# Optimization experiments

Measured on AMD Instinct MI355X. Metric: run time of the kernel, lower is better.

## Reference

```python
import jax, jax.numpy as jnp
import numpy as np

N_NODES = 100000
N_EDGES = 1600000
IN_SIZE = 256
OUT_SIZE = 64


def setup_inputs() -> dict:
    key = jax.random.key(0)
    k1, k2, k3 = jax.random.split(key, 3)
    edge_index = jax.random.randint(k1, (2, N_EDGES), 0, N_NODES, dtype=jnp.int32)
    x = jax.random.normal(k2, (N_NODES, IN_SIZE), dtype=jnp.float32)
    W = jax.random.normal(k3, (OUT_SIZE, IN_SIZE), dtype=jnp.float32) * 0.05
    return {"edge_index": edge_index, "x": x, "num_nodes": N_NODES, "W": W}


def reference(edge_index, x, num_nodes, W):
    row, col = edge_index[0], edge_index[1]
    # fill_diag(adj, 1.0): drop any existing diagonal entries (value -> 0),
    # then add exactly one self-loop per node with value 1.0.
    val = jnp.where(row == col, 0.0, 1.0).astype(x.dtype)
    loops = jnp.arange(num_nodes, dtype=row.dtype)
    row_f = jnp.concatenate([row, loops])
    col_f = jnp.concatenate([col, loops])
    val_f = jnp.concatenate([val, jnp.ones((num_nodes,), dtype=x.dtype)])
    # deg = row-sum of adjacency values; D^{-1/2} with inf -> 0
    deg = jax.ops.segment_sum(val_f, row_f, num_segments=num_nodes)
    dinv = jnp.where(deg > 0, deg ** -0.5, 0.0)
    # edge weight: d^{-1/2}[row] * a * d^{-1/2}[col]
    norm = dinv[row_f] * val_f * dinv[col_f]
    # dense projection then SpMM aggregation
    xw = x @ W.T  # [N, out]
    msgs = norm[:, None] * xw[col_f]  # gather over edges [E+N, out]
    out = jax.ops.segment_sum(msgs, row_f, num_segments=num_nodes)
    return out
```

## Files before the change

kernel.cpp:

```cpp
#include <hip/hip_runtime.h>

#define IN_SIZE 256
#define OUT_SIZE 64
#define BSHIFT 7
#define BROWS 128
#define BMASK 127
#define CAP 2560
#define K1_TILE 4096

typedef __attribute__((ext_vector_type(8))) short short8;
typedef __attribute__((ext_vector_type(4))) float floatx4;

__device__ inline unsigned short f2bf(float f) {
  unsigned u = __builtin_bit_cast(unsigned, f);
  u += 0x7fff + ((u >> 16) & 1);
  return (unsigned short)(u >> 16);
}
__device__ inline float bf2f(unsigned short u) {
  unsigned v = (unsigned)u << 16;
  return __builtin_bit_cast(float, v);
}

__global__ __launch_bounds__(256) void wconv_kernel(const float* __restrict__ W,
                                                    unsigned short* __restrict__ Wb,
                                                    int* __restrict__ coarse_cursor,
                                                    int total, int nbuck) {
  int i = blockIdx.x * 256 + threadIdx.x;
  if (i < total) Wb[i] = f2bf(W[i]);
  if (i < nbuck) coarse_cursor[i] = 0;
}

__global__ __launch_bounds__(256) void bucket_coarse_kernel(
    const int* __restrict__ row, const int* __restrict__ col,
    int* __restrict__ coarse_cursor, unsigned* __restrict__ pairs,
    int n_edges, int nbuck) {
  __shared__ int hist[1024];
  int tid = threadIdx.x;
#pragma unroll
  for (int i = 0; i < 4; i++) hist[tid + i * 256] = 0;
  __syncthreads();

  int r[16], c[16];
  int ebase = blockIdx.x * K1_TILE + tid;
#pragma unroll
  for (int i = 0; i < 16; i++) {
    int e = ebase + i * 256;
    bool ok = e < n_edges;
    r[i] = ok ? row[e] : -1;
    c[i] = ok ? col[e] : -1;
    if (ok && r[i] != c[i]) atomicAdd(&hist[r[i] >> BSHIFT], 1);
  }
  __syncthreads();

  for (int i = tid; i < nbuck; i += 256) {
    int cnt = hist[i];
    if (cnt) hist[i] = atomicAdd(&coarse_cursor[i], cnt);
  }
  __syncthreads();

#pragma unroll
  for (int i = 0; i < 16; i++) {
    if (r[i] >= 0 && r[i] != c[i]) {
      int bin = r[i] >> BSHIFT;
      int slot = atomicAdd(&hist[bin], 1);
      if (slot < CAP)
        pairs[(size_t)bin * CAP + slot] =
            ((unsigned)(r[i] & BMASK) << 17) | (unsigned)c[i];
    }
  }
}

__global__ __launch_bounds__(256) void bucket_fine_kernel(
    const int* __restrict__ coarse_cursor, const unsigned* __restrict__ pairs,
    unsigned* __restrict__ colsp, int* __restrict__ count,
    int* __restrict__ row_start, float* __restrict__ dinv, int n_nodes) {
  __shared__ unsigned lpair[CAP];
  __shared__ int hist[BROWS];
  __shared__ int scn[BROWS];
  int tid = threadIdx.x;
  int b = blockIdx.x;
  size_t base = (size_t)b * CAP;
  int n_b = coarse_cursor[b];
  if (n_b > CAP) n_b = CAP;

  if (tid < BROWS) hist[tid] = 0;
  __syncthreads();

  for (int i = tid; i < n_b; i += 256) {
    unsigned p = pairs[base + i];
    lpair[i] = p;
    atomicAdd(&hist[p >> 17], 1);
  }
  __syncthreads();

  if (tid < BROWS) scn[tid] = hist[tid];
  __syncthreads();
  for (int off = 1; off < BROWS; off <<= 1) {
    int t = (tid >= off && tid < BROWS) ? scn[tid - off] : 0;
    __syncthreads();
    if (tid < BROWS) scn[tid] += t;
    __syncthreads();
  }

  if (tid < BROWS) {
    int e = (tid > 0) ? scn[tid - 1] : 0;
    int r = b * BROWS + tid;
    if (r < n_nodes) {
      int deg = hist[tid];
      count[r] = deg;
      row_start[r] = (int)base + e;
      dinv[r] = rsqrtf((float)deg + 1.0f);
    }
    hist[tid] = e;
  }
  __syncthreads();

  for (int i = tid; i < n_b; i += 256) {
    unsigned p = lpair[i];
    int slot = atomicAdd(&hist[p >> 17], 1);
    colsp[base + slot] = p & 0x1FFFFu;
  }
}

#define WPAD 264
__global__ __launch_bounds__(512) void matmul_kernel(
    const float* __restrict__ x, const unsigned short* __restrict__ Wb,
    const float* __restrict__ dinv, unsigned short* __restrict__ xwd,
    int n_nodes) {
  __shared__ unsigned short w_lds[64][WPAD];

  int tid = threadIdx.x;
  int wave = tid >> 6;
  int lane = tid & 63;
  int quad = lane >> 4;
  int lcol = lane & 15;
  long nbase = (long)blockIdx.x * 128;

  {
    int r = tid >> 3;
    int q = tid & 7;
    const unsigned short* src = Wb + (size_t)r * IN_SIZE + q * 32;
#pragma unroll
    for (int i = 0; i < 4; i++)
      *(short8*)(&w_lds[r][q * 32 + i * 8]) = *(const short8*)(src + i * 8);
  }
  __syncthreads();

  long node = nbase + wave * 16 + lcol;
  long nclamp = (node < (long)n_nodes) ? node : (long)(n_nodes - 1);
  const float* xrow = x + nclamp * IN_SIZE;

  floatx4 acc[4];
#pragma unroll
  for (int t = 0; t < 4; t++) acc[t] = (floatx4){0.f, 0.f, 0.f, 0.f};

#pragma unroll
  for (int kk = 0; kk < 8; kk++) {
    const float* p = xrow + kk * 32 + quad * 8;
    float4 a = *(const float4*)(p);
    float4 bb = *(const float4*)(p + 4);
    short8 bfrag;
    bfrag[0] = (short)f2bf(a.x);  bfrag[1] = (short)f2bf(a.y);
    bfrag[2] = (short)f2bf(a.z);  bfrag[3] = (short)f2bf(a.w);
    bfrag[4] = (short)f2bf(bb.x); bfrag[5] = (short)f2bf(bb.y);
    bfrag[6] = (short)f2bf(bb.z); bfrag[7] = (short)f2bf(bb.w);
#pragma unroll
    for (int t = 0; t < 4; t++) {
      short8 afrag = *(const short8*)(&w_lds[t * 16 + lcol][kk * 32 + quad * 8]);
      acc[t] =
          __builtin_amdgcn_mfma_f32_16x16x32_bf16(afrag, bfrag, acc[t], 0, 0, 0);
    }
  }

  if (node < (long)n_nodes) {
    float dv = dinv[node];
#pragma unroll
    for (int t = 0; t < 4; t++) {
      ushort4 sv;
      sv.x = f2bf(dv * acc[t][0]);
      sv.y = f2bf(dv * acc[t][1]);
      sv.z = f2bf(dv * acc[t][2]);
      sv.w = f2bf(dv * acc[t][3]);
      *(ushort4*)(xwd + node * OUT_SIZE + t * 16 + quad * 4) = sv;
    }
  }
}

__global__ __launch_bounds__(256) void gather_kernel(
    const int* __restrict__ row_start, const int* __restrict__ count,
    const unsigned* __restrict__ colsp, const float* __restrict__ dinv,
    const unsigned short* __restrict__ xwd, float* __restrict__ out,
    int n_nodes) {
  int lane = threadIdx.x & 63;
  int wave = threadIdx.x >> 6;
  int sub = lane & 7;
  int cg = lane >> 3;
  int rb = (blockIdx.x * 4 + wave) * 4;
  if (rb >= n_nodes) return;

  int start[4], cnt[4];
  int maxc = 0;
#pragma unroll
  for (int i = 0; i < 4; i++) {
    int r = rb + i;
    bool ok = r < n_nodes;
    start[i] = ok ? row_start[r] : 0;
    cnt[i] = ok ? count[r] : 0;
    maxc = max(maxc, cnt[i]);
  }

  float acc[4][8];
#pragma unroll
  for (int i = 0; i < 4; i++)
#pragma unroll
    for (int k = 0; k < 8; k++) acc[i][k] = 0.f;

  if (sub == 0) {
#pragma unroll
    for (int i = 0; i < 4; i++) {
      int r = rb + i;
      if (r < n_nodes) {
        short8 v = *(const short8*)(xwd + (size_t)r * OUT_SIZE + cg * 8);
#pragma unroll
        for (int k = 0; k < 8; k++) acc[i][k] = bf2f((unsigned short)v[k]);
      }
    }
  }

  for (int j = 0; j < maxc; j += 8) {
    int c[4];
    float m[4];
    int idx = j + sub;
#pragma unroll
    for (int i = 0; i < 4; i++) {
      bool act = idx < cnt[i];
      c[i] = act ? (int)colsp[start[i] + idx] : rb;
      m[i] = act ? 1.0f : 0.0f;
    }
    short8 v[4];
#pragma unroll
    for (int i = 0; i < 4; i++)
      v[i] = *(const short8*)(xwd + (size_t)c[i] * OUT_SIZE + cg * 8);
#pragma unroll
    for (int i = 0; i < 4; i++)
#pragma unroll
      for (int k = 0; k < 8; k++)
        acc[i][k] += m[i] * bf2f((unsigned short)v[i][k]);
  }

#pragma unroll
  for (int i = 0; i < 4; i++)
#pragma unroll
    for (int k = 0; k < 8; k++) {
      acc[i][k] += __shfl_xor(acc[i][k], 1);
      acc[i][k] += __shfl_xor(acc[i][k], 2);
      acc[i][k] += __shfl_xor(acc[i][k], 4);
    }

  if (sub == 0) {
#pragma unroll
    for (int i = 0; i < 4; i++) {
      int r = rb + i;
      if (r < n_nodes) {
        float dr = dinv[r];
        float* dst = out + (size_t)r * OUT_SIZE + cg * 8;
        *(float4*)(dst) =
            make_float4(dr * acc[i][0], dr * acc[i][1], dr * acc[i][2],
                        dr * acc[i][3]);
        *(float4*)(dst + 4) =
            make_float4(dr * acc[i][4], dr * acc[i][5], dr * acc[i][6],
                        dr * acc[i][7]);
      }
    }
  }
}

extern "C" void kernel_launch(void* const* d_in, const int* in_sizes, int n_in,
                              void* d_out, int out_size, void* d_ws,
                              size_t ws_size, hipStream_t stream) {
  const int* edge_index = (const int*)d_in[0];
  const float* x = (const float*)d_in[1];
  const float* W = (const float*)d_in[3];

  int n_edges = in_sizes[0] / 2;
  int n_nodes = in_sizes[1] / IN_SIZE;
  const int* row = edge_index;
  const int* col = edge_index + n_edges;
  float* out = (float*)d_out;

  int nbuck = (n_nodes + BROWS - 1) >> BSHIFT;

  char* ws = (char*)d_ws;
  size_t nb = ((size_t)n_nodes * 4 + 15) & ~(size_t)15;
  int* count = (int*)ws;
  int* row_start = (int*)(ws + nb);
  float* dinv = (float*)(ws + 2 * nb);
  int* coarse_cursor = (int*)(ws + 3 * nb);
  size_t bucketsB = (size_t)nbuck * CAP * 4;
  unsigned* pairs = (unsigned*)(ws + 3 * nb + 4096);
  unsigned* colsp = (unsigned*)(ws + 3 * nb + 4096 + bucketsB);
  unsigned short* xwd =
      (unsigned short*)(ws + 3 * nb + 4096 + 2 * bucketsB);
  unsigned short* Wb =
      (unsigned short*)(ws + 3 * nb + 4096 + 2 * bucketsB +
                        (size_t)n_nodes * OUT_SIZE * 2);

  wconv_kernel<<<(OUT_SIZE * IN_SIZE + 255) / 256, 256, 0, stream>>>(
      W, Wb, coarse_cursor, OUT_SIZE * IN_SIZE, nbuck);
  int nb1 = (n_edges + K1_TILE - 1) / K1_TILE;
  bucket_coarse_kernel<<<nb1, 256, 0, stream>>>(row, col, coarse_cursor,
                                                pairs, n_edges, nbuck);
  bucket_fine_kernel<<<nbuck, 256, 0, stream>>>(coarse_cursor, pairs, colsp,
                                                count, row_start, dinv,
                                                n_nodes);
  matmul_kernel<<<(n_nodes + 127) / 128, 512, 0, stream>>>(x, Wb, dinv, xwd,
                                                           n_nodes);
  gather_kernel<<<(n_nodes + 15) / 16, 256, 0, stream>>>(
      row_start, count, colsp, dinv, xwd, out, n_nodes);
}
```

Baseline: 266.7 us.

## Fuse bucketing with matmul and fine-sort with gather to cut launches

Cuts the pipeline from five kernels to three. The coarse edge bucketing and the bf16 MFMA projection now run as disjoint block ranges of one launch, and each thread converts W to bf16 itself. The fine per-row sort and the aggregation are merged so sorted column indices stay in LDS instead of round-tripping through global memory. Degrees are now counted with a global atomic per edge and the D^{-1/2} scale is recomputed per gathered neighbour, which adds atomic traffic and an extra random count load per edge in exchange for fewer launches and less memory traffic.

```diff
diff --git a/kernel.cpp b/kernel.cpp
--- a/kernel.cpp
+++ b/kernel.cpp
@@ -6,7 +6,8 @@
 #define BROWS 128
 #define BMASK 127
 #define CAP 2560
-#define K1_TILE 4096
+#define K1_EDGES 8192
+#define WPAD 264
 
 typedef __attribute__((ext_vector_type(8))) short short8;
 typedef __attribute__((ext_vector_type(4))) float floatx4;
@@ -21,62 +22,143 @@
   return __builtin_bit_cast(float, v);
 }
 
-__global__ __launch_bounds__(256) void wconv_kernel(const float* __restrict__ W,
-                                                    unsigned short* __restrict__ Wb,
-                                                    int* __restrict__ coarse_cursor,
-                                                    int total, int nbuck) {
-  int i = blockIdx.x * 256 + threadIdx.x;
-  if (i < total) Wb[i] = f2bf(W[i]);
-  if (i < nbuck) coarse_cursor[i] = 0;
-}
-
-__global__ __launch_bounds__(256) void bucket_coarse_kernel(
+__global__ __launch_bounds__(512) void zero_kernel(int* __restrict__ count,
+                                                   int* __restrict__ cursor,
+                                                   int n_nodes) {
+  int i = blockIdx.x * 512 + threadIdx.x;
+  if (i < n_nodes) count[i] = 0;
+  if (i < 1024) cursor[i] = 0;
+}
+
+struct K1SM {
+  union {
+    int hist[1024];
+    unsigned short w[64 * WPAD];
+  };
+};
+
+__global__ __launch_bounds__(512) void fused1_kernel(
     const int* __restrict__ row, const int* __restrict__ col,
     int* __restrict__ coarse_cursor, unsigned* __restrict__ pairs,
-    int n_edges, int nbuck) {
-  __shared__ int hist[1024];
+    int* __restrict__ count, const float* __restrict__ x,
+    const float* __restrict__ W, unsigned short* __restrict__ xwb,
+    int n_edges, int n_nodes, int nbuck, int nb_coarse) {
+  __shared__ K1SM sm;
   int tid = threadIdx.x;
-#pragma unroll
-  for (int i = 0; i < 4; i++) hist[tid + i * 256] = 0;
-  __syncthreads();
-
-  int r[16], c[16];
-  int ebase = blockIdx.x * K1_TILE + tid;
-#pragma unroll
-  for (int i = 0; i < 16; i++) {
-    int e = ebase + i * 256;
-    bool ok = e < n_edges;
-    r[i] = ok ? row[e] : -1;
-    c[i] = ok ? col[e] : -1;
-    if (ok && r[i] != c[i]) atomicAdd(&hist[r[i] >> BSHIFT], 1);
-  }
-  __syncthreads();
-
-  for (int i = tid; i < nbuck; i += 256) {
-    int cnt = hist[i];
-    if (cnt) hist[i] = atomicAdd(&coarse_cursor[i], cnt);
-  }
-  __syncthreads();
-
-#pragma unroll
-  for (int i = 0; i < 16; i++) {
-    if (r[i] >= 0 && r[i] != c[i]) {
-      int bin = r[i] >> BSHIFT;
-      int slot = atomicAdd(&hist[bin], 1);
-      if (slot < CAP)
-        pairs[(size_t)bin * CAP + slot] =
-            ((unsigned)(r[i] & BMASK) << 17) | (unsigned)c[i];
-    }
-  }
-}
-
-__global__ __launch_bounds__(256) void bucket_fine_kernel(
+  int bid = blockIdx.x;
+
+  if (bid < nb_coarse) {
+    sm.hist[tid] = 0;
+    sm.hist[tid + 512] = 0;
+    __syncthreads();
+
+    int r[16], c[16];
+    int ebase = bid * K1_EDGES + tid;
+#pragma unroll
+    for (int i = 0; i < 16; i++) {
+      int e = ebase + i * 512;
+      bool ok = e < n_edges;
+      r[i] = ok ? row[e] : -1;
+      c[i] = ok ? col[e] : -1;
+      if (ok && r[i] != c[i]) {
+        atomicAdd(&sm.hist[r[i] >> BSHIFT], 1);
+        atomicAdd(&count[r[i]], 1);
+      }
+    }
+    __syncthreads();
+
+    for (int i = tid; i < nbuck; i += 512) {
+      int cnt = sm.hist[i];
+      if (cnt) sm.hist[i] = atomicAdd(&coarse_cursor[i], cnt);
+    }
+    __syncthreads();
+
+#pragma unroll
+    for (int i = 0; i < 16; i++) {
+      if (r[i] >= 0 && r[i] != c[i]) {
+        int bin = r[i] >> BSHIFT;
+        int slot = atomicAdd(&sm.hist[bin], 1);
+        if (slot < CAP)
+          pairs[(size_t)bin * CAP + slot] =
+              ((unsigned)(r[i] & BMASK) << 17) | (unsigned)c[i];
+      }
+    }
+  } else {
+    int mb = bid - nb_coarse;
+    long nbase = (long)mb * 128;
+    {
+      int r = tid >> 3;
+      int q = tid & 7;
+      const float* src = W + (size_t)r * IN_SIZE + q * 32;
+#pragma unroll
+      for (int i = 0; i < 4; i++) {
+        float4 a = *(const float4*)(src + i * 8);
+        float4 b = *(const float4*)(src + i * 8 + 4);
+        short8 s;
+        s[0] = (short)f2bf(a.x); s[1] = (short)f2bf(a.y);
+        s[2] = (short)f2bf(a.z); s[3] = (short)f2bf(a.w);
+        s[4] = (short)f2bf(b.x); s[5] = (short)f2bf(b.y);
+        s[6] = (short)f2bf(b.z); s[7] = (short)f2bf(b.w);
+        *(short8*)(&sm.w[r * WPAD + q * 32 + i * 8]) = s;
+      }
+    }
+    __syncthreads();
+
+    int wave = tid >> 6;
+    int lane = tid & 63;
+    int quad = lane >> 4;
+    int lcol = lane & 15;
+    long node = nbase + wave * 16 + lcol;
+    long nclamp = (node < (long)n_nodes) ? node : (long)(n_nodes - 1);
+    const float* xrow = x + nclamp * IN_SIZE;
+
+    floatx4 acc[4];
+#pragma unroll
+    for (int t = 0; t < 4; t++) acc[t] = (floatx4){0.f, 0.f, 0.f, 0.f};
+
+#pragma unroll
+    for (int kk = 0; kk < 8; kk++) {
+      const float* p = xrow + kk * 32 + quad * 8;
+      float4 a = *(const float4*)(p);
+      float4 bb = *(const float4*)(p + 4);
+      short8 bfrag;
+      bfrag[0] = (short)f2bf(a.x);  bfrag[1] = (short)f2bf(a.y);
+      bfrag[2] = (short)f2bf(a.z);  bfrag[3] = (short)f2bf(a.w);
+      bfrag[4] = (short)f2bf(bb.x); bfrag[5] = (short)f2bf(bb.y);
+      bfrag[6] = (short)f2bf(bb.z); bfrag[7] = (short)f2bf(bb.w);
+#pragma unroll
+      for (int t = 0; t < 4; t++) {
+        short8 afrag =
+            *(const short8*)(&sm.w[(t * 16 + lcol) * WPAD + kk * 32 + quad * 8]);
+        acc[t] = __builtin_amdgcn_mfma_f32_16x16x32_bf16(afrag, bfrag, acc[t],
+                                                         0, 0, 0);
+      }
+    }
+
+    if (node < (long)n_nodes) {
+#pragma unroll
+      for (int t = 0; t < 4; t++) {
+        ushort4 sv;
+        sv.x = f2bf(acc[t][0]);
+        sv.y = f2bf(acc[t][1]);
+        sv.z = f2bf(acc[t][2]);
+        sv.w = f2bf(acc[t][3]);
+        *(ushort4*)(xwb + node * OUT_SIZE + t * 16 + quad * 4) = sv;
+      }
+    }
+  }
+}
+
+__global__ __launch_bounds__(512) void fused2_kernel(
     const int* __restrict__ coarse_cursor, const unsigned* __restrict__ pairs,
-    unsigned* __restrict__ colsp, int* __restrict__ count,
-    int* __restrict__ row_start, float* __restrict__ dinv, int n_nodes) {
+    const int* __restrict__ count, const unsigned short* __restrict__ xwb,
+    float* __restrict__ out, int n_nodes) {
   __shared__ unsigned lpair[CAP];
+  __shared__ unsigned lcol[CAP];
   __shared__ int hist[BROWS];
-  __shared__ int scn[BROWS];
+  __shared__ int rs[BROWS];
+  __shared__ int cur[BROWS];
+
   int tid = threadIdx.x;
   int b = blockIdx.x;
   size_t base = (size_t)b * CAP;
@@ -86,190 +168,114 @@
   if (tid < BROWS) hist[tid] = 0;
   __syncthreads();
 
-  for (int i = tid; i < n_b; i += 256) {
+  for (int i = tid; i < n_b; i += 512) {
     unsigned p = pairs[base + i];
     lpair[i] = p;
     atomicAdd(&hist[p >> 17], 1);
   }
   __syncthreads();
 
-  if (tid < BROWS) scn[tid] = hist[tid];
+  if (tid < BROWS) rs[tid] = hist[tid];
   __syncthreads();
   for (int off = 1; off < BROWS; off <<= 1) {
-    int t = (tid >= off && tid < BROWS) ? scn[tid - off] : 0;
-    __syncthreads();
-    if (tid < BROWS) scn[tid] += t;
-    __syncthreads();
-  }
-
+    int t = (tid >= off && tid < BROWS) ? rs[tid - off] : 0;
+    __syncthreads();
+    if (tid < BROWS) rs[tid] += t;
+    __syncthreads();
+  }
   if (tid < BROWS) {
-    int e = (tid > 0) ? scn[tid - 1] : 0;
-    int r = b * BROWS + tid;
-    if (r < n_nodes) {
-      int deg = hist[tid];
-      count[r] = deg;
-      row_start[r] = (int)base + e;
-      dinv[r] = rsqrtf((float)deg + 1.0f);
-    }
-    hist[tid] = e;
-  }
-  __syncthreads();
-
-  for (int i = tid; i < n_b; i += 256) {
+    int ex = rs[tid] - hist[tid];
+    rs[tid] = ex;
+    cur[tid] = ex;
+  }
+  __syncthreads();
+
+  for (int i = tid; i < n_b; i += 512) {
     unsigned p = lpair[i];
-    int slot = atomicAdd(&hist[p >> 17], 1);
-    colsp[base + slot] = p & 0x1FFFFu;
-  }
-}
-
-#define WPAD 264
-__global__ __launch_bounds__(512) void matmul_kernel(
-    const float* __restrict__ x, const unsigned short* __restrict__ Wb,
-    const float* __restrict__ dinv, unsigned short* __restrict__ xwd,
-    int n_nodes) {
-  __shared__ unsigned short w_lds[64][WPAD];
-
-  int tid = threadIdx.x;
+    int slot = atomicAdd(&cur[p >> 17], 1);
+    lcol[slot] = p & 0x1FFFFu;
+  }
+  __syncthreads();
+
   int wave = tid >> 6;
   int lane = tid & 63;
-  int quad = lane >> 4;
-  int lcol = lane & 15;
-  long nbase = (long)blockIdx.x * 128;
-
-  {
-    int r = tid >> 3;
-    int q = tid & 7;
-    const unsigned short* src = Wb + (size_t)r * IN_SIZE + q * 32;
-#pragma unroll
-    for (int i = 0; i < 4; i++)
-      *(short8*)(&w_lds[r][q * 32 + i * 8]) = *(const short8*)(src + i * 8);
-  }
-  __syncthreads();
-
-  long node = nbase + wave * 16 + lcol;
-  long nclamp = (node < (long)n_nodes) ? node : (long)(n_nodes - 1);
-  const float* xrow = x + nclamp * IN_SIZE;
-
-  floatx4 acc[4];
-#pragma unroll
-  for (int t = 0; t < 4; t++) acc[t] = (floatx4){0.f, 0.f, 0.f, 0.f};
-
-#pragma unroll
-  for (int kk = 0; kk < 8; kk++) {
-    const float* p = xrow + kk * 32 + quad * 8;
-    float4 a = *(const float4*)(p);
-    float4 bb = *(const float4*)(p + 4);
-    short8 bfrag;
-    bfrag[0] = (short)f2bf(a.x);  bfrag[1] = (short)f2bf(a.y);
-    bfrag[2] = (short)f2bf(a.z);  bfrag[3] = (short)f2bf(a.w);
-    bfrag[4] = (short)f2bf(bb.x); bfrag[5] = (short)f2bf(bb.y);
-    bfrag[6] = (short)f2bf(bb.z); bfrag[7] = (short)f2bf(bb.w);
-#pragma unroll
-    for (int t = 0; t < 4; t++) {
-      short8 afrag = *(const short8*)(&w_lds[t * 16 + lcol][kk * 32 + quad * 8]);
-      acc[t] =
-          __builtin_amdgcn_mfma_f32_16x16x32_bf16(afrag, bfrag, acc[t], 0, 0, 0);
-    }
-  }
-
-  if (node < (long)n_nodes) {
-    float dv = dinv[node];
-#pragma unroll
-    for (int t = 0; t < 4; t++) {
-      ushort4 sv;
-      sv.x = f2bf(dv * acc[t][0]);
-      sv.y = f2bf(dv * acc[t][1]);
-      sv.z = f2bf(dv * acc[t][2]);
-      sv.w = f2bf(dv * acc[t][3]);
-      *(ushort4*)(xwd + node * OUT_SIZE + t * 16 + quad * 4) = sv;
-    }
-  }
-}
-
-__global__ __launch_bounds__(256) void gather_kernel(
-    const int* __restrict__ row_start, const int* __restrict__ count,
-    const unsigned* __restrict__ colsp, const float* __restrict__ dinv,
-    const unsigned short* __restrict__ xwd, float* __restrict__ out,
-    int n_nodes) {
-  int lane = threadIdx.x & 63;
-  int wave = threadIdx.x >> 6;
   int sub = lane & 7;
   int cg = lane >> 3;
-  int rb = (blockIdx.x * 4 + wave) * 4;
-  if (rb >= n_nodes) return;
-
-  int start[4], cnt[4];
-  int maxc = 0;
-#pragma unroll
-  for (int i = 0; i < 4; i++) {
-    int r = rb + i;
-    bool ok = r < n_nodes;
-    start[i] = ok ? row_start[r] : 0;
-    cnt[i] = ok ? count[r] : 0;
-    maxc = max(maxc, cnt[i]);
-  }
-
-  float acc[4][8];
-#pragma unroll
-  for (int i = 0; i < 4; i++)
-#pragma unroll
-    for (int k = 0; k < 8; k++) acc[i][k] = 0.f;
-
-  if (sub == 0) {
+
+  for (int g = 0; g < 4; g++) {
+    int rl = wave * 16 + g * 4;
+    int s4[4], c4[4];
+    int maxc = 0;
 #pragma unroll
     for (int i = 0; i < 4; i++) {
-      int r = rb + i;
-      if (r < n_nodes) {
-        short8 v = *(const short8*)(xwd + (size_t)r * OUT_SIZE + cg * 8);
-#pragma unroll
-        for (int k = 0; k < 8; k++) acc[i][k] = bf2f((unsigned short)v[k]);
-      }
-    }
-  }
-
-  for (int j = 0; j < maxc; j += 8) {
-    int c[4];
-    float m[4];
-    int idx = j + sub;
-#pragma unroll
-    for (int i = 0; i < 4; i++) {
-      bool act = idx < cnt[i];
-      c[i] = act ? (int)colsp[start[i] + idx] : rb;
-      m[i] = act ? 1.0f : 0.0f;
-    }
-    short8 v[4];
+      s4[i] = rs[rl + i];
+      c4[i] = hist[rl + i];
+      maxc = max(maxc, c4[i]);
+    }
+
+    float acc[4][8];
 #pragma unroll
     for (int i = 0; i < 4; i++)
-      v[i] = *(const short8*)(xwd + (size_t)c[i] * OUT_SIZE + cg * 8);
+#pragma unroll
+      for (int k = 0; k < 8; k++) acc[i][k] = 0.f;
+
+    if (sub == 0) {
+#pragma unroll
+      for (int i = 0; i < 4; i++) {
+        int r = b * BROWS + rl + i;
+        if (r < n_nodes) {
+          float dv = rsqrtf((float)count[r] + 1.0f);
+          short8 v = *(const short8*)(xwb + (size_t)r * OUT_SIZE + cg * 8);
+#pragma unroll
+          for (int k = 0; k < 8; k++) acc[i][k] = dv * bf2f((unsigned short)v[k]);
+        }
+      }
+    }
+
+    for (int j = 0; j < maxc; j += 8) {
+      int idx = j + sub;
+      int cc[4];
+      float m[4];
+#pragma unroll
+      for (int i = 0; i < 4; i++) {
+        bool act = idx < c4[i];
+        cc[i] = act ? (int)lcol[s4[i] + idx] : 0;
+        m[i] = act ? rsqrtf((float)count[cc[i]] + 1.0f) : 0.f;
+      }
+      short8 v[4];
+#pragma unroll
+      for (int i = 0; i < 4; i++)
+        v[i] = *(const short8*)(xwb + (size_t)cc[i] * OUT_SIZE + cg * 8);
+#pragma unroll
+      for (int i = 0; i < 4; i++)
+#pragma unroll
+        for (int k = 0; k < 8; k++)
+          acc[i][k] += m[i] * bf2f((unsigned short)v[i][k]);
+    }
+
 #pragma unroll
     for (int i = 0; i < 4; i++)
 #pragma unroll
-      for (int k = 0; k < 8; k++)
-        acc[i][k] += m[i] * bf2f((unsigned short)v[i][k]);
-  }
-
-#pragma unroll
-  for (int i = 0; i < 4; i++)
-#pragma unroll
-    for (int k = 0; k < 8; k++) {
-      acc[i][k] += __shfl_xor(acc[i][k], 1);
-      acc[i][k] += __shfl_xor(acc[i][k], 2);
-      acc[i][k] += __shfl_xor(acc[i][k], 4);
-    }
-
-  if (sub == 0) {
-#pragma unroll
-    for (int i = 0; i < 4; i++) {
-      int r = rb + i;
-      if (r < n_nodes) {
-        float dr = dinv[r];
-        float* dst = out + (size_t)r * OUT_SIZE + cg * 8;
-        *(float4*)(dst) =
-            make_float4(dr * acc[i][0], dr * acc[i][1], dr * acc[i][2],
-                        dr * acc[i][3]);
-        *(float4*)(dst + 4) =
-            make_float4(dr * acc[i][4], dr * acc[i][5], dr * acc[i][6],
-                        dr * acc[i][7]);
+      for (int k = 0; k < 8; k++) {
+        acc[i][k] += __shfl_xor(acc[i][k], 1);
+        acc[i][k] += __shfl_xor(acc[i][k], 2);
+        acc[i][k] += __shfl_xor(acc[i][k], 4);
+      }
+
+    if (sub == 0) {
+#pragma unroll
+      for (int i = 0; i < 4; i++) {
+        int r = b * BROWS + rl + i;
+        if (r < n_nodes) {
+          float dr = rsqrtf((float)count[r] + 1.0f);
+          float* dst = out + (size_t)r * OUT_SIZE + cg * 8;
+          *(float4*)(dst) =
+              make_float4(dr * acc[i][0], dr * acc[i][1], dr * acc[i][2],
+                          dr * acc[i][3]);
+          *(float4*)(dst + 4) =
+              make_float4(dr * acc[i][4], dr * acc[i][5], dr * acc[i][6],
+                          dr * acc[i][7]);
+        }
       }
     }
   }
@@ -289,32 +295,22 @@
   float* out = (float*)d_out;
 
   int nbuck = (n_nodes + BROWS - 1) >> BSHIFT;
+  int nb_coarse = (n_edges + K1_EDGES - 1) / K1_EDGES;
+  int nb_mm = (n_nodes + 127) / 128;
 
   char* ws = (char*)d_ws;
-  size_t nb = ((size_t)n_nodes * 4 + 15) & ~(size_t)15;
+  size_t nb4 = ((size_t)n_nodes * 4 + 15) & ~(size_t)15;
   int* count = (int*)ws;
-  int* row_start = (int*)(ws + nb);
-  float* dinv = (float*)(ws + 2 * nb);
-  int* coarse_cursor = (int*)(ws + 3 * nb);
-  size_t bucketsB = (size_t)nbuck * CAP * 4;
-  unsigned* pairs = (unsigned*)(ws + 3 * nb + 4096);
-  unsigned* colsp = (unsigned*)(ws + 3 * nb + 4096 + bucketsB);
-  unsigned short* xwd =
-      (unsigned short*)(ws + 3 * nb + 4096 + 2 * bucketsB);
-  unsigned short* Wb =
-      (unsigned short*)(ws + 3 * nb + 4096 + 2 * bucketsB +
-                        (size_t)n_nodes * OUT_SIZE * 2);
-
-  wconv_kernel<<<(OUT_SIZE * IN_SIZE + 255) / 256, 256, 0, stream>>>(
-      W, Wb, coarse_cursor, OUT_SIZE * IN_SIZE, nbuck);
-  int nb1 = (n_edges + K1_TILE - 1) / K1_TILE;
-  bucket_coarse_kernel<<<nb1, 256, 0, stream>>>(row, col, coarse_cursor,
-                                                pairs, n_edges, nbuck);
-  bucket_fine_kernel<<<nbuck, 256, 0, stream>>>(coarse_cursor, pairs, colsp,
-                                                count, row_start, dinv,
-                                                n_nodes);
-  matmul_kernel<<<(n_nodes + 127) / 128, 512, 0, stream>>>(x, Wb, dinv, xwd,
-                                                           n_nodes);
-  gather_kernel<<<(n_nodes + 15) / 16, 256, 0, stream>>>(
-      row_start, count, colsp, dinv, xwd, out, n_nodes);
-}
+  int* coarse_cursor = (int*)(ws + nb4);
+  unsigned* pairs = (unsigned*)(ws + nb4 + 4096);
+  size_t pairsB = (size_t)nbuck * CAP * 4;
+  unsigned short* xwb = (unsigned short*)(ws + nb4 + 4096 + pairsB);
+
+  zero_kernel<<<(n_nodes + 511) / 512, 512, 0, stream>>>(count, coarse_cursor,
+                                                         n_nodes);
+  fused1_kernel<<<nb_coarse + nb_mm, 512, 0, stream>>>(
+      row, col, coarse_cursor, pairs, count, x, W, xwb, n_edges, n_nodes,
+      nbuck, nb_coarse);
+  fused2_kernel<<<nbuck, 512, 0, stream>>>(coarse_cursor, pairs, count, xwb,
+                                           out, n_nodes);
+}
```

After: 311.0 us. +16.6%, slower.
